# Optimization experiments

Hardware: AMD Instinct MI355X
Metric: run time of the kernel (lower is better)

## Reference

```python
import jax, jax.numpy as jnp
import numpy as np

B, IN, H = 8192, 1024, 1024

def setup_inputs() -> dict:
    key = jax.random.key(0)
    ks = jax.random.split(key, 12)
    s_i = 1.0 / np.sqrt(IN)   # lecun-normal-ish scale for input kernels
    s_h = 1.0 / np.sqrt(H)
    d = {
        'inputs': jax.random.normal(ks[0], (B, IN), jnp.float32),
        'c': jax.random.normal(ks[1], (B, H), jnp.float32),
        'h': jax.random.normal(ks[2], (B, H), jnp.float32),
    }
    for n, k in zip(['Wii', 'Wif', 'Wig', 'Wio'], ks[3:7]):
        d[n] = jax.random.normal(k, (IN, H), jnp.float32) * s_i
    for n, k in zip(['Whi', 'Whf', 'Whg', 'Who'], ks[7:11]):
        d[n] = jax.random.normal(k, (H, H), jnp.float32) * s_h
    for n in ['bi', 'bf', 'bg', 'bo']:
        d[n] = jnp.zeros((H,), jnp.float32)
    return d

def reference(inputs, c, h, Wii, Wif, Wig, Wio, Whi, Whf, Whg, Who, bi, bf, bg, bo):
    # i = sigmoid(x Wii + h Whi + bi); f, o likewise; g = tanh(x Wig + h Whg + bg)
    i = jax.nn.sigmoid(inputs @ Wii + h @ Whi + bi)
    f = jax.nn.sigmoid(inputs @ Wif + h @ Whf + bf)
    g = jnp.tanh(inputs @ Wig + h @ Whg + bg)
    o = jax.nn.sigmoid(inputs @ Wio + h @ Who + bo)
    new_c = f * c + i * g
    new_h = o * jnp.tanh(new_c)
    return (new_c, new_h)
```

## Files before the change

### kernel.cpp

```cpp
#include <hip/hip_runtime.h>
#include <hip/hip_bf16.h>
#include <cstdint>


#define B_DIM 8192
#define H_DIM 1024
#define K2    2048
#define N4    4096
#define BK    64
#define BM    128
#define BN    256

typedef __bf16 bf16x8 __attribute__((ext_vector_type(8)));
typedef float  f32x16 __attribute__((ext_vector_type(16)));

__device__ __forceinline__ void async_load16(const __bf16* g, __bf16* l) {
  __builtin_amdgcn_global_load_lds(
      (__attribute__((address_space(1))) void*)(g),
      (__attribute__((address_space(3))) void*)(l),
      16, 0, 0);
}

__device__ __forceinline__ float sigm(float x) {
  return 1.0f / (1.0f + __expf(-x));
}
__device__ __forceinline__ float tanh_fast(float x) {
  return 2.0f / (1.0f + __expf(-2.0f * x)) - 1.0f;
}

__global__ void cast_a(const float* __restrict__ x, const float* __restrict__ h,
                       __bf16* __restrict__ A) {
  int row = blockIdx.x;
  int k = threadIdx.x << 3;
  const float* src = (k < H_DIM) ? (x + (size_t)row * H_DIM + k)
                                 : (h + (size_t)row * H_DIM + (k - H_DIM));
  float4 v0 = *(const float4*)src;
  float4 v1 = *(const float4*)(src + 4);
  bf16x8 o;
  o[0] = (__bf16)v0.x; o[1] = (__bf16)v0.y; o[2] = (__bf16)v0.z; o[3] = (__bf16)v0.w;
  o[4] = (__bf16)v1.x; o[5] = (__bf16)v1.y; o[6] = (__bf16)v1.z; o[7] = (__bf16)v1.w;
  *(bf16x8*)&A[(size_t)row * K2 + k] = o;
}

__global__ void cast_w(const float* __restrict__ Wii, const float* __restrict__ Wif,
                       const float* __restrict__ Wig, const float* __restrict__ Wio,
                       const float* __restrict__ Whi, const float* __restrict__ Whf,
                       const float* __restrict__ Whg, const float* __restrict__ Who,
                       __bf16* __restrict__ Bt2) {
  __shared__ float tile[64][33];
  int k0 = blockIdx.x * 64;
  int jg = blockIdx.y;
  int j0 = jg * 32;
  int gate = blockIdx.z;
  const float* Wi[4] = {Wii, Wif, Wig, Wio};
  const float* Wh[4] = {Whi, Whf, Whg, Who};
  const float* W = (k0 < H_DIM) ? Wi[gate] : Wh[gate];
  int kb = (k0 < H_DIM) ? k0 : (k0 - H_DIM);

  int col = threadIdx.x & 31;
  int rr  = threadIdx.x >> 5;
#pragma unroll
  for (int p = 0; p < 8; ++p)
    tile[p * 8 + rr][col] = W[(size_t)(kb + p * 8 + rr) * H_DIM + j0 + col];
  __syncthreads();

  int jj = threadIdx.x & 31;
  int kq = threadIdx.x >> 5;
  int kt = (k0 >> 4) + (kq >> 1);
  int h8 = kq & 1;
  bf16x8 o;
#pragma unroll
  for (int e = 0; e < 8; ++e) o[e] = (__bf16)tile[kq * 8 + e][jj];
  size_t chunk = ((size_t)jg * 128 + kt) * 4 + gate;
  *(bf16x8*)&Bt2[chunk * 512 + (h8 * 32 + jj) * 8] = o;
}

__global__ __launch_bounds__(256, 2) void lstm_gemm(
    const __bf16* __restrict__ A,
    const __bf16* __restrict__ Bt2,
    const float* __restrict__ c,
    const float* __restrict__ bi, const float* __restrict__ bf_,
    const float* __restrict__ bg, const float* __restrict__ bo,
    float* __restrict__ out_c, float* __restrict__ out_h) {
  __shared__ __align__(16) __bf16 As[2][BM * BK];

  const int tid  = threadIdx.x;
  const int wave = tid >> 6;
  const int lane = tid & 63;
  const int wm   = wave >> 1;
  const int wn   = wave & 1;
  const int m0   = blockIdx.x * BM;
  const int jg   = blockIdx.y * 2 + wn;

  f32x16 acc[2][4] = {};

  const int l31 = lane & 31;
  const int h8  = lane >> 5;

  const int rin  = lane >> 3;
  const int slot = lane & 7;
  const int sg   = slot ^ rin;
  const __bf16* gA[4];
  int lA[4];
#pragma unroll
  for (int cc = 0; cc < 4; ++cc) {
    int r = wave * 32 + cc * 8 + rin;
    gA[cc] = A + (size_t)(m0 + r) * K2 + sg * 8;
    lA[cc] = (wave * 4 + cc) * 512;
  }

  const __bf16* bbase = Bt2 + ((size_t)jg * 128 * 4) * 512 + lane * 8;

#pragma unroll
  for (int cc = 0; cc < 4; ++cc) async_load16(gA[cc], &As[0][lA[cc]]);

  for (int it = 0; it < K2 / BK; ++it) {
    const int k0 = it * BK;
    const int p  = it & 1;
    __syncthreads();
    if (it + 1 < K2 / BK) {
#pragma unroll
      for (int cc = 0; cc < 4; ++cc)
        async_load16(gA[cc] + k0 + BK, &As[p ^ 1][lA[cc]]);
    }

    const int kt0 = k0 >> 4;
#pragma unroll
    for (int ks = 0; ks < 4; ++ks) {
      bf16x8 bfr[4];
#pragma unroll
      for (int g = 0; g < 4; ++g)
        bfr[g] = *(const bf16x8*)(bbase + ((size_t)(kt0 + ks) * 4 + g) * 512);

      bf16x8 af[2];
      const int sw = ((ks * 2 + h8) ^ (l31 & 7)) * 8;
#pragma unroll
      for (int t = 0; t < 2; ++t)
        af[t] = *(const bf16x8*)&As[p][(wm * 64 + t * 32 + l31) * BK + sw];

#pragma unroll
      for (int tm = 0; tm < 2; ++tm)
#pragma unroll
        for (int g = 0; g < 4; ++g)
          acc[tm][g] = __builtin_amdgcn_mfma_f32_32x32x16_bf16(
              af[tm], bfr[g], acc[tm][g], 0, 0, 0);
    }
  }

  const int j = jg * 32 + l31;
  const float vbi = bi[j], vbf = bf_[j], vbg = bg[j], vbo = bo[j];

#pragma unroll
  for (int tm = 0; tm < 2; ++tm) {
#pragma unroll
    for (int r = 0; r < 16; ++r) {
      int row = m0 + wm * 64 + tm * 32 + 4 * h8 + (r & 3) + 8 * (r >> 2);
      float gi = sigm(acc[tm][0][r] + vbi);
      float gf = sigm(acc[tm][1][r] + vbf);
      float gg = tanh_fast(acc[tm][2][r] + vbg);
      float go = sigm(acc[tm][3][r] + vbo);
      size_t idx = (size_t)row * H_DIM + j;
      float cv = c[idx];
      float nc = gf * cv + gi * gg;
      float nh = go * tanh_fast(nc);
      out_c[idx] = nc;
      out_h[idx] = nh;
    }
  }
}

extern "C" void kernel_launch(void* const* d_in, const int* in_sizes, int n_in,
                              void* d_out, int out_size, void* d_ws, size_t ws_size,
                              hipStream_t stream) {
  const float* x   = (const float*)d_in[0];
  const float* c   = (const float*)d_in[1];
  const float* h   = (const float*)d_in[2];
  const float* Wii = (const float*)d_in[3];
  const float* Wif = (const float*)d_in[4];
  const float* Wig = (const float*)d_in[5];
  const float* Wio = (const float*)d_in[6];
  const float* Whi = (const float*)d_in[7];
  const float* Whf = (const float*)d_in[8];
  const float* Whg = (const float*)d_in[9];
  const float* Who = (const float*)d_in[10];
  const float* bi  = (const float*)d_in[11];
  const float* bf_ = (const float*)d_in[12];
  const float* bg  = (const float*)d_in[13];
  const float* bo  = (const float*)d_in[14];

  __bf16* Abf = (__bf16*)d_ws;
  __bf16* Bt2 = (__bf16*)((char*)d_ws + (size_t)B_DIM * K2 * 2);

  float* out_c = (float*)d_out;
  float* out_h = out_c + (size_t)B_DIM * H_DIM;

  cast_a<<<B_DIM, 256, 0, stream>>>(x, h, Abf);
  dim3 gw(K2 / 64, H_DIM / 32, 4);
  cast_w<<<gw, 256, 0, stream>>>(Wii, Wif, Wig, Wio, Whi, Whf, Whg, Who, Bt2);
  dim3 gg(B_DIM / BM, N4 / BN);
  lstm_gemm<<<gg, 256, 0, stream>>>(Abf, Bt2, c, bi, bf_, bg, bo, out_c, out_h);
}
```

Before: 361.7 us.

## Pre-pack A into MFMA fragment layout and drop LDS staging in GEMM

```diff
diff --git a/kernel.cpp b/kernel.cpp
--- a/kernel.cpp
+++ b/kernel.cpp
@@ -7,19 +7,10 @@
 #define H_DIM 1024
 #define K2    2048
 #define N4    4096
-#define BK    64
-#define BM    128
-#define BN    256
+#define NKT   (K2 / 16)
 
 typedef __bf16 bf16x8 __attribute__((ext_vector_type(8)));
 typedef float  f32x16 __attribute__((ext_vector_type(16)));
-
-__device__ __forceinline__ void async_load16(const __bf16* g, __bf16* l) {
-  __builtin_amdgcn_global_load_lds(
-      (__attribute__((address_space(1))) void*)(g),
-      (__attribute__((address_space(3))) void*)(l),
-      16, 0, 0);
-}
 
 __device__ __forceinline__ float sigm(float x) {
   return 1.0f / (1.0f + __expf(-x));
@@ -29,17 +20,20 @@
 }
 
 __global__ void cast_a(const float* __restrict__ x, const float* __restrict__ h,
-                       __bf16* __restrict__ A) {
-  int row = blockIdx.x;
-  int k = threadIdx.x << 3;
-  const float* src = (k < H_DIM) ? (x + (size_t)row * H_DIM + k)
-                                 : (h + (size_t)row * H_DIM + (k - H_DIM));
+                       __bf16* __restrict__ Af) {
+  int r = blockIdx.x;
+  int t = threadIdx.x;
+  int k = t << 3;
+  const float* src = (k < H_DIM) ? (x + (size_t)r * H_DIM + k)
+                                 : (h + (size_t)r * H_DIM + (k - H_DIM));
   float4 v0 = *(const float4*)src;
   float4 v1 = *(const float4*)(src + 4);
   bf16x8 o;
   o[0] = (__bf16)v0.x; o[1] = (__bf16)v0.y; o[2] = (__bf16)v0.z; o[3] = (__bf16)v0.w;
   o[4] = (__bf16)v1.x; o[5] = (__bf16)v1.y; o[6] = (__bf16)v1.z; o[7] = (__bf16)v1.w;
-  *(bf16x8*)&A[(size_t)row * K2 + k] = o;
+  size_t addr = (((size_t)(r >> 5) * NKT + (t >> 1)) * 512) +
+                ((size_t)((t & 1) * 32 + (r & 31))) * 8;
+  *(bf16x8*)&Af[addr] = o;
 }
 
 __global__ void cast_w(const float* __restrict__ Wii, const float* __restrict__ Wif,
@@ -71,82 +65,65 @@
   bf16x8 o;
 #pragma unroll
   for (int e = 0; e < 8; ++e) o[e] = (__bf16)tile[kq * 8 + e][jj];
-  size_t chunk = ((size_t)jg * 128 + kt) * 4 + gate;
+  size_t chunk = ((size_t)jg * NKT + kt) * 4 + gate;
   *(bf16x8*)&Bt2[chunk * 512 + (h8 * 32 + jj) * 8] = o;
 }
 
 __global__ __launch_bounds__(256, 2) void lstm_gemm(
-    const __bf16* __restrict__ A,
+    const __bf16* __restrict__ Af,
     const __bf16* __restrict__ Bt2,
     const float* __restrict__ c,
     const float* __restrict__ bi, const float* __restrict__ bf_,
     const float* __restrict__ bg, const float* __restrict__ bo,
     float* __restrict__ out_c, float* __restrict__ out_h) {
-  __shared__ __align__(16) __bf16 As[2][BM * BK];
-
   const int tid  = threadIdx.x;
   const int wave = tid >> 6;
   const int lane = tid & 63;
   const int wm   = wave >> 1;
   const int wn   = wave & 1;
-  const int m0   = blockIdx.x * BM;
   const int jg   = blockIdx.y * 2 + wn;
+  const int mg0  = blockIdx.x * 4 + wm * 2;
 
   f32x16 acc[2][4] = {};
 
+  const __bf16* pA0 = Af  + ((size_t)(mg0 + 0) * NKT) * 512 + lane * 8;
+  const __bf16* pA1 = Af  + ((size_t)(mg0 + 1) * NKT) * 512 + lane * 8;
+  const __bf16* pB  = Bt2 + ((size_t)jg * NKT * 4) * 512 + lane * 8;
+
+  bf16x8 a0[2], b0[4], a1[2], b1[4];
+  a0[0] = *(const bf16x8*)(pA0);
+  a0[1] = *(const bf16x8*)(pA1);
+#pragma unroll
+  for (int g = 0; g < 4; ++g) b0[g] = *(const bf16x8*)(pB + g * 512);
+
+#pragma unroll 2
+  for (int kt = 0; kt < NKT - 1; ++kt) {
+    a1[0] = *(const bf16x8*)(pA0 + (size_t)(kt + 1) * 512);
+    a1[1] = *(const bf16x8*)(pA1 + (size_t)(kt + 1) * 512);
+#pragma unroll
+    for (int g = 0; g < 4; ++g)
+      b1[g] = *(const bf16x8*)(pB + ((size_t)(kt + 1) * 4 + g) * 512);
+
+#pragma unroll
+    for (int tm = 0; tm < 2; ++tm)
+#pragma unroll
+      for (int g = 0; g < 4; ++g)
+        acc[tm][g] = __builtin_amdgcn_mfma_f32_32x32x16_bf16(
+            a0[tm], b0[g], acc[tm][g], 0, 0, 0);
+
+    a0[0] = a1[0]; a0[1] = a1[1];
+#pragma unroll
+    for (int g = 0; g < 4; ++g) b0[g] = b1[g];
+  }
+#pragma unroll
+  for (int tm = 0; tm < 2; ++tm)
+#pragma unroll
+    for (int g = 0; g < 4; ++g)
+      acc[tm][g] = __builtin_amdgcn_mfma_f32_32x32x16_bf16(
+          a0[tm], b0[g], acc[tm][g], 0, 0, 0);
+
   const int l31 = lane & 31;
   const int h8  = lane >> 5;
-
-  const int rin  = lane >> 3;
-  const int slot = lane & 7;
-  const int sg   = slot ^ rin;
-  const __bf16* gA[4];
-  int lA[4];
-#pragma unroll
-  for (int cc = 0; cc < 4; ++cc) {
-    int r = wave * 32 + cc * 8 + rin;
-    gA[cc] = A + (size_t)(m0 + r) * K2 + sg * 8;
-    lA[cc] = (wave * 4 + cc) * 512;
-  }
-
-  const __bf16* bbase = Bt2 + ((size_t)jg * 128 * 4) * 512 + lane * 8;
-
-#pragma unroll
-  for (int cc = 0; cc < 4; ++cc) async_load16(gA[cc], &As[0][lA[cc]]);
-
-  for (int it = 0; it < K2 / BK; ++it) {
-    const int k0 = it * BK;
-    const int p  = it & 1;
-    __syncthreads();
-    if (it + 1 < K2 / BK) {
-#pragma unroll
-      for (int cc = 0; cc < 4; ++cc)
-        async_load16(gA[cc] + k0 + BK, &As[p ^ 1][lA[cc]]);
-    }
-
-    const int kt0 = k0 >> 4;
-#pragma unroll
-    for (int ks = 0; ks < 4; ++ks) {
-      bf16x8 bfr[4];
-#pragma unroll
-      for (int g = 0; g < 4; ++g)
-        bfr[g] = *(const bf16x8*)(bbase + ((size_t)(kt0 + ks) * 4 + g) * 512);
-
-      bf16x8 af[2];
-      const int sw = ((ks * 2 + h8) ^ (l31 & 7)) * 8;
-#pragma unroll
-      for (int t = 0; t < 2; ++t)
-        af[t] = *(const bf16x8*)&As[p][(wm * 64 + t * 32 + l31) * BK + sw];
-
-#pragma unroll
-      for (int tm = 0; tm < 2; ++tm)
-#pragma unroll
-        for (int g = 0; g < 4; ++g)
-          acc[tm][g] = __builtin_amdgcn_mfma_f32_32x32x16_bf16(
-              af[tm], bfr[g], acc[tm][g], 0, 0, 0);
-    }
-  }
-
   const int j = jg * 32 + l31;
   const float vbi = bi[j], vbf = bf_[j], vbg = bg[j], vbo = bo[j];
 
@@ -154,7 +131,7 @@
   for (int tm = 0; tm < 2; ++tm) {
 #pragma unroll
     for (int r = 0; r < 16; ++r) {
-      int row = m0 + wm * 64 + tm * 32 + 4 * h8 + (r & 3) + 8 * (r >> 2);
+      int row = (mg0 + tm) * 32 + 4 * h8 + (r & 3) + 8 * (r >> 2);
       float gi = sigm(acc[tm][0][r] + vbi);
       float gf = sigm(acc[tm][1][r] + vbf);
       float gg = tanh_fast(acc[tm][2][r] + vbg);
@@ -188,15 +165,15 @@
   const float* bg  = (const float*)d_in[13];
   const float* bo  = (const float*)d_in[14];
 
-  __bf16* Abf = (__bf16*)d_ws;
+  __bf16* Af  = (__bf16*)d_ws;
   __bf16* Bt2 = (__bf16*)((char*)d_ws + (size_t)B_DIM * K2 * 2);
 
   float* out_c = (float*)d_out;
   float* out_h = out_c + (size_t)B_DIM * H_DIM;
 
-  cast_a<<<B_DIM, 256, 0, stream>>>(x, h, Abf);
+  cast_a<<<B_DIM, 256, 0, stream>>>(x, h, Af);
   dim3 gw(K2 / 64, H_DIM / 32, 4);
   cast_w<<<gw, 256, 0, stream>>>(Wii, Wif, Wig, Wio, Whi, Whf, Whg, Who, Bt2);
-  dim3 gg(B_DIM / BM, N4 / BN);
-  lstm_gemm<<<gg, 256, 0, stream>>>(Abf, Bt2, c, bi, bf_, bg, bo, out_c, out_h);
+  dim3 gg(B_DIM / 128, N4 / 256);
+  lstm_gemm<<<gg, 256, 0, stream>>>(Af, Bt2, c, bi, bf_, bg, bo, out_c, out_h);
 }
```

After: 424.5 us. +17.4%, slower.
